# Kernel optimization log

Measured on AMD Instinct MI355X. Metric: run time of the kernel, lower is better.

The kernel has to match this reference:

```python
import jax, jax.numpy as jnp
import numpy as np

N = 50000      # nodes
E = 640000     # edges
F_IN = 64      # node feature dim
H = 128        # hidden channels
G = 256        # graphs in batch
NEG_SLOPE = 0.2
BN_EPS = 1e-5


def setup_inputs() -> dict:
    key = jax.random.key(0)
    ks = jax.random.split(key, 32)
    rn = lambda k, shape, s=0.1: jax.random.normal(k, shape, dtype=jnp.float32) * s
    inp = {
        'x': jax.random.normal(ks[0], (N, F_IN), dtype=jnp.float32),
        'edge_index': jax.random.randint(ks[1], (2, E), 0, N, dtype=jnp.int32),
        'batch': jnp.sort(jax.random.randint(ks[2], (N,), 0, G, dtype=jnp.int32)),
        # GATConv 1
        'W1': rn(ks[3], (F_IN, H)), 'as1': rn(ks[4], (H,)), 'ad1': rn(ks[5], (H,)), 'b1': jnp.zeros((H,), jnp.float32),
        # GATConv 2
        'W2': rn(ks[6], (H, H)), 'as2': rn(ks[7], (H,)), 'ad2': rn(ks[8], (H,)), 'b2': jnp.zeros((H,), jnp.float32),
        # GATConv 3
        'W3': rn(ks[9], (H, H)), 'as3': rn(ks[10], (H,)), 'ad3': rn(ks[11], (H,)), 'b3': jnp.zeros((H,), jnp.float32),
        # BatchNorm (inference: running stats)
        'g1': jnp.ones((H,), jnp.float32), 'be1': jnp.zeros((H,), jnp.float32), 'm1': rn(ks[12], (H,), 0.01), 'v1': jnp.ones((H,), jnp.float32),
        'g2': jnp.ones((H,), jnp.float32), 'be2': jnp.zeros((H,), jnp.float32), 'm2': rn(ks[13], (H,), 0.01), 'v2': jnp.ones((H,), jnp.float32),
        'g3': jnp.ones((H,), jnp.float32), 'be3': jnp.zeros((H,), jnp.float32), 'm3': rn(ks[14], (H,), 0.01), 'v3': jnp.ones((H,), jnp.float32),
        # MLP head
        'lw1': rn(ks[15], (H, H)), 'lb1': jnp.zeros((H,), jnp.float32),
        'lw2': rn(ks[16], (H, 1)), 'lb2': jnp.zeros((1,), jnp.float32),
    }
    return inp


def gat_layer(x, src, dst, W, a_src, a_dst, b, n):
    # PyG GATConv, heads=1: linear, per-edge attention, segment softmax over dst, scatter-add.
    h = x @ W                                  # [N, H]
    s_src = h @ a_src                          # [N]
    s_dst = h @ a_dst                          # [N]
    e = jax.nn.leaky_relu(s_src[src] + s_dst[dst], NEG_SLOPE)   # [E']
    m = jax.ops.segment_max(e, dst, num_segments=n)
    ex = jnp.exp(e - m[dst])
    denom = jax.ops.segment_sum(ex, dst, num_segments=n)
    coef = ex / denom[dst]                     # softmax per destination node
    out = jax.ops.segment_sum(coef[:, None] * h[src], dst, num_segments=n)
    return out + b


def batch_norm(x, g, b, mean, var):
    return (x - mean) * jax.lax.rsqrt(var + BN_EPS) * g + b


def reference(x, edge_index, batch,
              W1, as1, ad1, b1, W2, as2, ad2, b2, W3, as3, ad3, b3,
              g1, be1, m1, v1, g2, be2, m2, v2, g3, be3, m3, v3,
              lw1, lb1, lw2, lb2):
    n = x.shape[0]
    loops = jnp.arange(n, dtype=edge_index.dtype)      # PyG adds self-loops by default
    src = jnp.concatenate([edge_index[0], loops])
    dst = jnp.concatenate([edge_index[1], loops])

    h = gat_layer(x, src, dst, W1, as1, ad1, b1, n)
    h = jax.nn.relu(batch_norm(h, g1, be1, m1, v1))
    h = gat_layer(h, src, dst, W2, as2, ad2, b2, n)
    h = jax.nn.relu(batch_norm(h, g2, be2, m2, v2))
    h = gat_layer(h, src, dst, W3, as3, ad3, b3, n)
    h = jax.nn.relu(batch_norm(h, g3, be3, m3, v3))

    # global_mean_pool
    counts = jax.ops.segment_sum(jnp.ones((n,), h.dtype), batch, num_segments=G)
    pooled = jax.ops.segment_sum(h, batch, num_segments=G) / jnp.maximum(counts, 1.0)[:, None]

    out = jax.nn.relu(pooled @ lw1 + lb1)
    out = out @ lw2 + lb2                               # [G, 1]
    return out
```

## Files before the change

kernel.cpp:

```cpp
#include <hip/hip_runtime.h>

#define HD 128
#define NEG 0.2f
#define BNEPS 1e-5f

typedef unsigned int uint32;
typedef __attribute__((ext_vector_type(8))) short short8;
typedef __attribute__((ext_vector_type(4))) float floatx4;


__device__ inline float wave_max_f(float v) {
#pragma unroll
  for (int off = 32; off; off >>= 1) v = fmaxf(v, __shfl_xor(v, off, 64));
  return v;
}
__device__ inline float wave_sum_f(float v) {
#pragma unroll
  for (int off = 32; off; off >>= 1) v += __shfl_xor(v, off, 64);
  return v;
}
__device__ inline int wave_sum_i(int v) {
#pragma unroll
  for (int off = 32; off; off >>= 1) v += __shfl_xor(v, off, 64);
  return v;
}
__device__ inline int wave_iscan_i(int v, int lane) {
#pragma unroll
  for (int off = 1; off < 64; off <<= 1) {
    int t = __shfl_up(v, off, 64);
    if (lane >= off) v += t;
  }
  return v;
}
__device__ inline uint32 f2bf(float f) {
  uint32 u = __float_as_uint(f);
  return (u + 0x7fffu + ((u >> 16) & 1u)) >> 16;
}
__device__ inline void kpair(int kc, int lg, int e2, bool perm, int& k_lo, int& k_hi) {
  if (!perm) {
    k_lo = kc * 32 + lg * 8 + e2 * 2;
    k_hi = k_lo + 1;
  } else {
    int w = kc * 16 + lg * 4 + e2;
    k_lo = ((w >> 4) << 5) + (w & 15);
    k_hi = k_lo + 16;
  }
}


__global__ void k_hist(const int* __restrict__ dst, int* __restrict__ deg, int E) {
  int i = blockIdx.x * blockDim.x + threadIdx.x;
  if (i < E) atomicAdd(&deg[dst[i]], 1);
}

__global__ __launch_bounds__(256) void k_scan_part(const int* __restrict__ deg,
                                                   int* __restrict__ part, int n) {
  const int t = threadIdx.x, lane = t & 63, wave = t >> 6;
  const int i = blockIdx.x * 256 + t;
  int v = (i < n) ? (deg[i] + 1) : 0;
  int wv = wave_sum_i(v);
  __shared__ int ws[4];
  if (lane == 0) ws[wave] = wv;
  __syncthreads();
  if (t == 0) part[blockIdx.x] = ws[0] + ws[1] + ws[2] + ws[3];
}

__global__ __launch_bounds__(256) void k_scan_part2(int* __restrict__ part, int nb) {
  const int t = threadIdx.x, lane = t & 63, wave = t >> 6;
  int v = (t < nb) ? part[t] : 0;
  int x = wave_iscan_i(v, lane);
  __shared__ int ws[4];
  if (lane == 63) ws[wave] = x;
  __syncthreads();
  int add = 0;
#pragma unroll
  for (int w = 0; w < 4; ++w)
    if (w < wave) add += ws[w];
  x += add;
  if (t < nb) part[t] = x;
}

__global__ __launch_bounds__(256) void k_scan_final(const int* __restrict__ deg,
                                                    const int* __restrict__ part,
                                                    int* __restrict__ offs,
                                                    int* __restrict__ csr,
                                                    int* __restrict__ cursor, int n) {
  const int t = threadIdx.x, lane = t & 63, wave = t >> 6;
  const int b = blockIdx.x;
  const int i = b * 256 + t;
  int v = (i < n) ? (deg[i] + 1) : 0;
  int x = wave_iscan_i(v, lane);
  __shared__ int ws[4];
  if (lane == 63) ws[wave] = x;
  __syncthreads();
  int add = (b > 0) ? part[b - 1] : 0;
#pragma unroll
  for (int w = 0; w < 4; ++w)
    if (w < wave) add += ws[w];
  x += add;
  if (i < n) {
    const int excl = x - v;
    offs[i + 1] = x;
    csr[excl] = i;
    cursor[i] = excl + 1;
  }
  if (i == 0) offs[0] = 0;
}

__global__ void k_fill_edges(const int* __restrict__ src, const int* __restrict__ dst,
                             int* __restrict__ cursor, int* __restrict__ csr, int E) {
  int i = blockIdx.x * blockDim.x + threadIdx.x;
  if (i < E) { int p = atomicAdd(&cursor[dst[i]], 1); csr[p] = src[i]; }
}

__global__ __launch_bounds__(256)
void k_pack(const float* __restrict__ W1, const float* __restrict__ as1v,
            const float* __restrict__ ad1v, const float* __restrict__ W2,
            const float* __restrict__ as2v, const float* __restrict__ ad2v,
            const float* __restrict__ W3, const float* __restrict__ as3v,
            const float* __restrict__ ad3v, uint32* __restrict__ PW1,
            uint32* __restrict__ PW2, uint32* __restrict__ PW3,
            uint32* __restrict__ BFA1, uint32* __restrict__ BFA2,
            uint32* __restrict__ BFA3) {
  const int b = blockIdx.x, t = threadIdx.x;
  if (b < 80) {
    const float* W;
    uint32* PW;
    int KC, local;
    bool perm;
    if (b < 16) { W = W1; PW = PW1; KC = 2; perm = false; local = b; }
    else if (b < 48) { W = W2; PW = PW2; KC = 4; perm = true; local = b - 16; }
    else { W = W3; PW = PW3; KC = 4; perm = true; local = b - 48; }
    const int idx = local * 256 + t;
    const int e2 = idx & 3, l = (idx >> 2) & 63, f = idx >> 8;
    const int kc = f % KC, ct = f / KC;
    int k_lo, k_hi;
    kpair(kc, l >> 4, e2, perm, k_lo, k_hi);
    const int col = ct * 16 + (l & 15);
    PW[idx] = f2bf(W[k_lo * HD + col]) | (f2bf(W[k_hi * HD + col]) << 16);
  } else {
    const int layer = b - 80;
    const float* W = layer == 0 ? W1 : layer == 1 ? W2 : W3;
    const float* av = layer == 0 ? as1v : layer == 1 ? as2v : as3v;
    const float* dv = layer == 0 ? ad1v : layer == 1 ? ad2v : ad3v;
    uint32* BFA = layer == 0 ? BFA1 : layer == 1 ? BFA2 : BFA3;
    const int K = layer == 0 ? 64 : 128, KC = K / 32;
    const bool perm = layer != 0;
    __shared__ float ws[128], wd[128];
    if (t < K) {
      float s = 0.f, d = 0.f;
      for (int j = 0; j < HD; ++j) {
        const float w = W[t * HD + j];
        s = fmaf(w, av[j], s);
        d = fmaf(w, dv[j], d);
      }
      ws[t] = s;
      wd[t] = d;
    }
    __syncthreads();
    const int total = KC * 256;
    for (int idx = t; idx < total; idx += 256) {
      const int e2 = idx & 3, l = (idx >> 2) & 63, kc = idx >> 8;
      int k_lo, k_hi;
      kpair(kc, l >> 4, e2, perm, k_lo, k_hi);
      const int li = l & 15;
      const float lo = li == 0 ? ws[k_lo] : li == 1 ? wd[k_lo] : 0.f;
      const float hi = li == 0 ? ws[k_hi] : li == 1 ? wd[k_hi] : 0.f;
      BFA[idx] = f2bf(lo) | (f2bf(hi) << 16);
    }
  }
}

template <int K, bool BF16IN>
__global__ __launch_bounds__(256)
void k_gemm_mfma(const void* __restrict__ Xv, const uint32* __restrict__ PW,
                 const uint32* __restrict__ BFA, uint32* __restrict__ Hh,
                 float* __restrict__ ssrc, float* __restrict__ sdst, int n) {
  constexpr int KC = K / 32;
  __shared__ uint32 Xl[64 * K / 2];
  const int t = threadIdx.x;
  const int wv = t >> 6, l = t & 63;
  const int rowbase = blockIdx.x * 64;

  short8 bfr[2][KC];
#pragma unroll
  for (int c2 = 0; c2 < 2; ++c2)
#pragma unroll
    for (int kc = 0; kc < KC; ++kc)
      bfr[c2][kc] = *((const short8*)PW + ((wv * 2 + c2) * KC + kc) * 64 + l);
  short8 bfa[KC];
  if (wv == 0) {
#pragma unroll
    for (int kc = 0; kc < KC; ++kc) bfa[kc] = *((const short8*)BFA + kc * 64 + l);
  }

  if (BF16IN) {
    const uint32* Xb = (const uint32*)Xv;
#pragma unroll
    for (int B = t; B < 64 * (K / 8); B += 256) {
      const int row = B / (K / 8), cb = B % (K / 8);
      const int r = min(rowbase + row, n - 1);
      const uint4 v = *(const uint4*)&Xb[(long)r * (K / 2) + cb * 4];
      *(uint4*)&Xl[row * (K / 2) + (cb ^ (row & 7)) * 4] = v;
    }
  } else {
    const float* X = (const float*)Xv;
    for (int i = t; i < 64 * (K / 4); i += 256) {
      const int row = i / (K / 4), kq = i % (K / 4);
      const int r = min(rowbase + row, n - 1);
      const float4 v = *(const float4*)&X[(long)r * K + kq * 4];
      uint2 p;
      p.x = f2bf(v.x) | (f2bf(v.y) << 16);
      p.y = f2bf(v.z) | (f2bf(v.w) << 16);
      int byte = row * (K * 2) + kq * 8;
      byte ^= (row & 7) << 4;
      *(uint2*)((char*)Xl + byte) = p;
    }
  }
  __syncthreads();

  floatx4 acc[4][2], acc2[4];
#pragma unroll
  for (int rt = 0; rt < 4; ++rt) {
    acc[rt][0] = (floatx4){0.f, 0.f, 0.f, 0.f};
    acc[rt][1] = (floatx4){0.f, 0.f, 0.f, 0.f};
    acc2[rt] = (floatx4){0.f, 0.f, 0.f, 0.f};
  }
  const int row_l = l & 15, kgrp = l >> 4;
#pragma unroll
  for (int rt = 0; rt < 4; ++rt) {
    const int row = rt * 16 + row_l;
#pragma unroll
    for (int kc = 0; kc < KC; ++kc) {
      const int byte = (row * (K * 2) + kc * 64 + kgrp * 16) ^ ((row & 7) << 4);
      const short8 af = *(const short8*)((const char*)Xl + byte);
      acc[rt][0] = __builtin_amdgcn_mfma_f32_16x16x32_bf16(af, bfr[0][kc], acc[rt][0], 0, 0, 0);
      acc[rt][1] = __builtin_amdgcn_mfma_f32_16x16x32_bf16(af, bfr[1][kc], acc[rt][1], 0, 0, 0);
      if (wv == 0)
        acc2[rt] = __builtin_amdgcn_mfma_f32_16x16x32_bf16(af, bfa[kc], acc2[rt], 0, 0, 0);
    }
  }

#pragma unroll
  for (int rt = 0; rt < 4; ++rt) {
#pragma unroll
    for (int r = 0; r < 4; ++r) {
      const int R = rowbase + rt * 16 + kgrp * 4 + r;
      if (R < n)
        Hh[(long)R * 64 + wv * 16 + row_l] =
            f2bf(acc[rt][0][r]) | (f2bf(acc[rt][1][r]) << 16);
    }
  }
  if (wv == 0 && row_l < 2) {
    float* tgt = (row_l == 0) ? ssrc : sdst;
#pragma unroll
    for (int rt = 0; rt < 4; ++rt)
#pragma unroll
      for (int r = 0; r < 4; ++r) {
        const int R = rowbase + rt * 16 + kgrp * 4 + r;
        if (R < n) tgt[R] = acc2[rt][r];
      }
  }
}

__global__ __launch_bounds__(256)
void k_agg(const uint32* __restrict__ Hh, const float* __restrict__ ssrc,
           const float* __restrict__ sdst, const int* __restrict__ offs,
           const int* __restrict__ csr, const float* __restrict__ bias,
           const float* __restrict__ gam, const float* __restrict__ bet,
           const float* __restrict__ mu, const float* __restrict__ var,
           uint32* __restrict__ Ybf, int n) {
  const int wid = (blockIdx.x * blockDim.x + threadIdx.x) >> 6;
  const int lane = threadIdx.x & 63;
  if (wid >= n) return;
  const int s0 = offs[wid], s1 = offs[wid + 1];
  const float sdv = sdst[wid];
  const int c0 = (lane >> 4) * 32 + (lane & 15);
  const int c1 = c0 + 16;
  float acc0 = 0.f, acc1 = 0.f, denom = 0.f, mx = -1e30f;
  for (int base = s0; base < s1; base += 64) {
    const int m = min(64, s1 - base);
    int sidx = 0;
    float e = -1e30f;
    if (lane < m) {
      sidx = csr[base + lane];
      float tt = ssrc[sidx] + sdv;
      e = (tt > 0.f) ? tt : NEG * tt;
    }
    const float cmx = wave_max_f(e);
    const float nmx = fmaxf(mx, cmx);
    if (nmx > mx) {
      const float sc = __expf(mx - nmx);
      acc0 *= sc; acc1 *= sc; denom *= sc;
      mx = nmx;
    }
    const float p = (lane < m) ? __expf(e - mx) : 0.f;
    denom += wave_sum_f(p);
    const uint32 pu = __float_as_uint(p);
    for (int jj = 0; jj < m; jj += 16) {
      int idxv[16];
      float wv[16];
#pragma unroll
      for (int u = 0; u < 16; ++u) {
        idxv[u] = __builtin_amdgcn_readlane(sidx, jj + u);
        wv[u] = __uint_as_float(__builtin_amdgcn_readlane(pu, jj + u));
      }
      uint32 g[16];
#pragma unroll
      for (int u = 0; u < 16; ++u) g[u] = Hh[(long)idxv[u] * 64 + lane];
#pragma unroll
      for (int u = 0; u < 16; ++u) {
        acc0 = fmaf(wv[u], __uint_as_float(g[u] << 16), acc0);
        acc1 = fmaf(wv[u], __uint_as_float(g[u] & 0xffff0000u), acc1);
      }
    }
  }
  const float inv = 1.f / denom;
  float v0 = acc0 * inv + bias[c0];
  float v1 = acc1 * inv + bias[c1];
  const float sc0 = gam[c0] * rsqrtf(var[c0] + BNEPS);
  const float sc1 = gam[c1] * rsqrtf(var[c1] + BNEPS);
  v0 = fmaxf((v0 - mu[c0]) * sc0 + bet[c0], 0.f);
  v1 = fmaxf((v1 - mu[c1]) * sc1 + bet[c1], 0.f);
  Ybf[(long)wid * 64 + lane] = f2bf(v0) | (f2bf(v1) << 16);
}

__global__ __launch_bounds__(256)
void k_pool_head(const uint32* __restrict__ Ybf, const int* __restrict__ batch, int n,
                 const float* __restrict__ lw1, const float* __restrict__ lb1,
                 const float* __restrict__ lw2, const float* __restrict__ lb2,
                 float* __restrict__ out) {
  const int g = blockIdx.x;
  const int wave = threadIdx.x >> 6, lane = threadIdx.x & 63;
  int lo = 0, hi = n;
  while (lo < hi) { int mid = (lo + hi) >> 1; if (batch[mid] < g) lo = mid + 1; else hi = mid; }
  const int start = lo;
  hi = n;
  while (lo < hi) { int mid = (lo + hi) >> 1; if (batch[mid] < g + 1) lo = mid + 1; else hi = mid; }
  const int end = lo;
  const int c0 = (lane >> 4) * 32 + (lane & 15);
  const int c1 = c0 + 16;
  float m0 = 0.f, m1 = 0.f;
  for (int i = start + wave; i < end; i += 4) {
    const uint32 gv = Ybf[(long)i * 64 + lane];
    m0 += __uint_as_float(gv << 16);
    m1 += __uint_as_float(gv & 0xffff0000u);
  }
  __shared__ float red[4][HD];
  red[wave][c0] = m0;
  red[wave][c1] = m1;
  __syncthreads();
  if (wave == 0) {
    m0 = red[0][c0] + red[1][c0] + red[2][c0] + red[3][c0];
    m1 = red[0][c1] + red[1][c1] + red[2][c1] + red[3][c1];
    const float cnt = (float)(end - start);
    const float invc = (cnt > 0.f) ? 1.f / cnt : 0.f;
    m0 *= invc;
    m1 *= invc;
    float t0 = lb1[c0], t1 = lb1[c1];
    for (int k = 0; k < HD; ++k) {
      const int srcl = ((k >> 5) << 4) + (k & 15);
      const float pv = __shfl(((k >> 4) & 1) ? m1 : m0, srcl, 64);
      t0 = fmaf(pv, lw1[k * HD + c0], t0);
      t1 = fmaf(pv, lw1[k * HD + c1], t1);
    }
    t0 = fmaxf(t0, 0.f);
    t1 = fmaxf(t1, 0.f);
    float p = t0 * lw2[c0] + t1 * lw2[c1];
#pragma unroll
    for (int off = 32; off; off >>= 1) p += __shfl_xor(p, off, 64);
    if (lane == 0) out[g] = p + lb2[0];
  }
}


extern "C" void kernel_launch(void* const* d_in, const int* in_sizes, int n_in,
                              void* d_out, int out_size, void* d_ws, size_t ws_size,
                              hipStream_t stream) {
  const float* x = (const float*)d_in[0];
  const int* ei = (const int*)d_in[1];
  const int* batch = (const int*)d_in[2];
  const float* W1 = (const float*)d_in[3];
  const float* as1 = (const float*)d_in[4];
  const float* ad1 = (const float*)d_in[5];
  const float* b1 = (const float*)d_in[6];
  const float* W2 = (const float*)d_in[7];
  const float* as2 = (const float*)d_in[8];
  const float* ad2 = (const float*)d_in[9];
  const float* b2 = (const float*)d_in[10];
  const float* W3 = (const float*)d_in[11];
  const float* as3 = (const float*)d_in[12];
  const float* ad3 = (const float*)d_in[13];
  const float* b3 = (const float*)d_in[14];
  const float* g1 = (const float*)d_in[15];
  const float* be1 = (const float*)d_in[16];
  const float* m1 = (const float*)d_in[17];
  const float* v1 = (const float*)d_in[18];
  const float* g2 = (const float*)d_in[19];
  const float* be2 = (const float*)d_in[20];
  const float* m2 = (const float*)d_in[21];
  const float* v2 = (const float*)d_in[22];
  const float* g3 = (const float*)d_in[23];
  const float* be3 = (const float*)d_in[24];
  const float* m3 = (const float*)d_in[25];
  const float* v3 = (const float*)d_in[26];
  const float* lw1 = (const float*)d_in[27];
  const float* lb1 = (const float*)d_in[28];
  const float* lw2 = (const float*)d_in[29];
  const float* lb2 = (const float*)d_in[30];

  const int n = in_sizes[0] / 64;
  const int E = in_sizes[1] / 2;
  const int* src = ei;
  const int* dst = ei + E;

  uint32* hbuf = (uint32*)d_ws;
  uint32* ybuf = hbuf + (long)n * 64;
  float* ssrc = (float*)(ybuf + (long)n * 64);
  float* sdstv = ssrc + n;
  int* deg = (int*)(sdstv + n);
  int* offs = deg + n;
  int* cursor = offs + n + 1;
  int* csr = cursor + n;
  int* part = csr + (E + n);
  uint32* PW1 = (uint32*)(part + 256);
  uint32* PW2 = PW1 + 4096;
  uint32* PW3 = PW2 + 8192;
  uint32* BFA1 = PW3 + 8192;
  uint32* BFA2 = BFA1 + 512;
  uint32* BFA3 = BFA2 + 1024;

  const int B = 256;
  dim3 blk(B);
  const int nb = (n + B - 1) / B;

  k_pack<<<dim3(83), blk, 0, stream>>>(W1, as1, ad1, W2, as2, ad2, W3, as3, ad3,
                                       PW1, PW2, PW3, BFA1, BFA2, BFA3);

  hipMemsetAsync(deg, 0, (size_t)n * sizeof(int), stream);
  k_hist<<<dim3((E + B - 1) / B), blk, 0, stream>>>(dst, deg, E);
  k_scan_part<<<dim3(nb), blk, 0, stream>>>(deg, part, n);
  k_scan_part2<<<dim3(1), blk, 0, stream>>>(part, nb);
  k_scan_final<<<dim3(nb), blk, 0, stream>>>(deg, part, offs, csr, cursor, n);
  k_fill_edges<<<dim3((E + B - 1) / B), blk, 0, stream>>>(src, dst, cursor, csr, E);

  const dim3 ggrid((n + 63) / 64);
  const dim3 agrid((n + 3) / 4);

  k_gemm_mfma<64, false><<<ggrid, blk, 0, stream>>>(x, PW1, BFA1, hbuf, ssrc, sdstv, n);
  k_agg<<<agrid, blk, 0, stream>>>(hbuf, ssrc, sdstv, offs, csr, b1, g1, be1, m1, v1, ybuf, n);
  k_gemm_mfma<128, true><<<ggrid, blk, 0, stream>>>(ybuf, PW2, BFA2, hbuf, ssrc, sdstv, n);
  k_agg<<<agrid, blk, 0, stream>>>(hbuf, ssrc, sdstv, offs, csr, b2, g2, be2, m2, v2, ybuf, n);
  k_gemm_mfma<128, true><<<ggrid, blk, 0, stream>>>(ybuf, PW3, BFA3, hbuf, ssrc, sdstv, n);
  k_agg<<<agrid, blk, 0, stream>>>(hbuf, ssrc, sdstv, offs, csr, b3, g3, be3, m3, v3, ybuf, n);

  k_pool_head<<<dim3(256), blk, 0, stream>>>(ybuf, batch, n, lw1, lb1, lw2, lb2,
                                             (float*)d_out);
}
```

Baseline: 242.6 us.

## Fuse CSR build into pack/GEMM launches and drop softmax max pass

Zeroing of degree counters moves into the weight-pack kernel, and the degree histogram runs as extra blocks of the first GEMM launch. The multi-kernel prefix scan is replaced by one kernel that allocates CSR segments with a global atomic, storing start/end pairs per node. The aggregation kernel drops the running-max softmax rescaling and exponentiates raw scores, and the gather loop is reorganized. This cuts launches and reduction work but risks exp overflow for large attention logits and changes CSR ordering.

```diff
diff --git a/kernel.cpp b/kernel.cpp
--- a/kernel.cpp
+++ b/kernel.cpp
@@ -9,17 +9,7 @@
 typedef __attribute__((ext_vector_type(4))) float floatx4;
 
 
-__device__ inline float wave_max_f(float v) {
-#pragma unroll
-  for (int off = 32; off; off >>= 1) v = fmaxf(v, __shfl_xor(v, off, 64));
-  return v;
-}
 __device__ inline float wave_sum_f(float v) {
-#pragma unroll
-  for (int off = 32; off; off >>= 1) v += __shfl_xor(v, off, 64);
-  return v;
-}
-__device__ inline int wave_sum_i(int v) {
 #pragma unroll
   for (int off = 32; off; off >>= 1) v += __shfl_xor(v, off, 64);
   return v;
@@ -47,72 +37,6 @@
   }
 }
 
-
-__global__ void k_hist(const int* __restrict__ dst, int* __restrict__ deg, int E) {
-  int i = blockIdx.x * blockDim.x + threadIdx.x;
-  if (i < E) atomicAdd(&deg[dst[i]], 1);
-}
-
-__global__ __launch_bounds__(256) void k_scan_part(const int* __restrict__ deg,
-                                                   int* __restrict__ part, int n) {
-  const int t = threadIdx.x, lane = t & 63, wave = t >> 6;
-  const int i = blockIdx.x * 256 + t;
-  int v = (i < n) ? (deg[i] + 1) : 0;
-  int wv = wave_sum_i(v);
-  __shared__ int ws[4];
-  if (lane == 0) ws[wave] = wv;
-  __syncthreads();
-  if (t == 0) part[blockIdx.x] = ws[0] + ws[1] + ws[2] + ws[3];
-}
-
-__global__ __launch_bounds__(256) void k_scan_part2(int* __restrict__ part, int nb) {
-  const int t = threadIdx.x, lane = t & 63, wave = t >> 6;
-  int v = (t < nb) ? part[t] : 0;
-  int x = wave_iscan_i(v, lane);
-  __shared__ int ws[4];
-  if (lane == 63) ws[wave] = x;
-  __syncthreads();
-  int add = 0;
-#pragma unroll
-  for (int w = 0; w < 4; ++w)
-    if (w < wave) add += ws[w];
-  x += add;
-  if (t < nb) part[t] = x;
-}
-
-__global__ __launch_bounds__(256) void k_scan_final(const int* __restrict__ deg,
-                                                    const int* __restrict__ part,
-                                                    int* __restrict__ offs,
-                                                    int* __restrict__ csr,
-                                                    int* __restrict__ cursor, int n) {
-  const int t = threadIdx.x, lane = t & 63, wave = t >> 6;
-  const int b = blockIdx.x;
-  const int i = b * 256 + t;
-  int v = (i < n) ? (deg[i] + 1) : 0;
-  int x = wave_iscan_i(v, lane);
-  __shared__ int ws[4];
-  if (lane == 63) ws[wave] = x;
-  __syncthreads();
-  int add = (b > 0) ? part[b - 1] : 0;
-#pragma unroll
-  for (int w = 0; w < 4; ++w)
-    if (w < wave) add += ws[w];
-  x += add;
-  if (i < n) {
-    const int excl = x - v;
-    offs[i + 1] = x;
-    csr[excl] = i;
-    cursor[i] = excl + 1;
-  }
-  if (i == 0) offs[0] = 0;
-}
-
-__global__ void k_fill_edges(const int* __restrict__ src, const int* __restrict__ dst,
-                             int* __restrict__ cursor, int* __restrict__ csr, int E) {
-  int i = blockIdx.x * blockDim.x + threadIdx.x;
-  if (i < E) { int p = atomicAdd(&cursor[dst[i]], 1); csr[p] = src[i]; }
-}
-
 __global__ __launch_bounds__(256)
 void k_pack(const float* __restrict__ W1, const float* __restrict__ as1v,
             const float* __restrict__ ad1v, const float* __restrict__ W2,
@@ -121,8 +45,15 @@
             const float* __restrict__ ad3v, uint32* __restrict__ PW1,
             uint32* __restrict__ PW2, uint32* __restrict__ PW3,
             uint32* __restrict__ BFA1, uint32* __restrict__ BFA2,
-            uint32* __restrict__ BFA3) {
+            uint32* __restrict__ BFA3, int* __restrict__ deg,
+            int* __restrict__ gcnt, int n) {
   const int b = blockIdx.x, t = threadIdx.x;
+  if (b >= 83) {
+    const int i = (b - 83) * 256 + t;
+    if (i < n) deg[i] = 0;
+    if (b == 83 && t == 0) gcnt[0] = 0;
+    return;
+  }
   if (b < 80) {
     const float* W;
     uint32* PW;
@@ -171,16 +102,49 @@
   }
 }
 
+__global__ __launch_bounds__(256)
+void k_alloc(const int* __restrict__ deg, int* __restrict__ gcnt,
+             int2* __restrict__ offs2, int* __restrict__ csr,
+             int* __restrict__ cursor, int n) {
+  const int t = threadIdx.x, lane = t & 63, wave = t >> 6;
+  const int i = blockIdx.x * 256 + t;
+  const int v = (i < n) ? deg[i] + 1 : 0;
+  const int x = wave_iscan_i(v, lane);
+  __shared__ int wsum[4];
+  __shared__ int bbase;
+  if (lane == 63) wsum[wave] = x;
+  __syncthreads();
+  if (t == 0) bbase = atomicAdd(gcnt, wsum[0] + wsum[1] + wsum[2] + wsum[3]);
+  __syncthreads();
+  int add = bbase;
+#pragma unroll
+  for (int w = 0; w < 4; ++w)
+    if (w < wave) add += wsum[w];
+  const int start = add + x - v;
+  if (i < n) {
+    offs2[i] = make_int2(start, start + v);
+    csr[start] = i;
+    cursor[i] = start + 1;
+  }
+}
+
+__global__ void k_fill_edges(const int* __restrict__ src, const int* __restrict__ dst,
+                             int* __restrict__ cursor, int* __restrict__ csr, int E) {
+  int i = blockIdx.x * blockDim.x + threadIdx.x;
+  if (i < E) { int p = atomicAdd(&cursor[dst[i]], 1); csr[p] = src[i]; }
+}
+
 template <int K, bool BF16IN>
-__global__ __launch_bounds__(256)
-void k_gemm_mfma(const void* __restrict__ Xv, const uint32* __restrict__ PW,
-                 const uint32* __restrict__ BFA, uint32* __restrict__ Hh,
-                 float* __restrict__ ssrc, float* __restrict__ sdst, int n) {
+__device__ inline void gemm_body(int bid, const void* __restrict__ Xv,
+                                 const uint32* __restrict__ PW,
+                                 const uint32* __restrict__ BFA,
+                                 uint32* __restrict__ Hh, float* __restrict__ ssrc,
+                                 float* __restrict__ sdst, int n) {
   constexpr int KC = K / 32;
   __shared__ uint32 Xl[64 * K / 2];
   const int t = threadIdx.x;
   const int wv = t >> 6, l = t & 63;
-  const int rowbase = blockIdx.x * 64;
+  const int rowbase = bid * 64;
 
   short8 bfr[2][KC];
 #pragma unroll
@@ -264,8 +228,30 @@
 }
 
 __global__ __launch_bounds__(256)
+void k_gemm1_hist(const void* __restrict__ Xv, const uint32* __restrict__ PW,
+                  const uint32* __restrict__ BFA, uint32* __restrict__ Hh,
+                  float* __restrict__ ssrc, float* __restrict__ sdst, int n,
+                  const int* __restrict__ dst, int* __restrict__ deg, int E, int GB) {
+  const int b = blockIdx.x;
+  if (b < GB) {
+    gemm_body<64, false>(b, Xv, PW, BFA, Hh, ssrc, sdst, n);
+  } else {
+    const int i = (b - GB) * 256 + threadIdx.x;
+    if (i < E) atomicAdd(&deg[dst[i]], 1);
+  }
+}
+
+template <int K>
+__global__ __launch_bounds__(256)
+void k_gemm_mfma(const void* __restrict__ Xv, const uint32* __restrict__ PW,
+                 const uint32* __restrict__ BFA, uint32* __restrict__ Hh,
+                 float* __restrict__ ssrc, float* __restrict__ sdst, int n) {
+  gemm_body<K, true>(blockIdx.x, Xv, PW, BFA, Hh, ssrc, sdst, n);
+}
+
+__global__ __launch_bounds__(256)
 void k_agg(const uint32* __restrict__ Hh, const float* __restrict__ ssrc,
-           const float* __restrict__ sdst, const int* __restrict__ offs,
+           const float* __restrict__ sdst, const int2* __restrict__ offs2,
            const int* __restrict__ csr, const float* __restrict__ bias,
            const float* __restrict__ gam, const float* __restrict__ bet,
            const float* __restrict__ mu, const float* __restrict__ var,
@@ -273,45 +259,39 @@
   const int wid = (blockIdx.x * blockDim.x + threadIdx.x) >> 6;
   const int lane = threadIdx.x & 63;
   if (wid >= n) return;
-  const int s0 = offs[wid], s1 = offs[wid + 1];
+  const int2 se = offs2[wid];
   const float sdv = sdst[wid];
   const int c0 = (lane >> 4) * 32 + (lane & 15);
   const int c1 = c0 + 16;
-  float acc0 = 0.f, acc1 = 0.f, denom = 0.f, mx = -1e30f;
-  for (int base = s0; base < s1; base += 64) {
-    const int m = min(64, s1 - base);
+  float acc0 = 0.f, acc1 = 0.f, denom = 0.f;
+  for (int base = se.x; base < se.y; base += 64) {
+    const int m = min(64, se.y - base);
     int sidx = 0;
-    float e = -1e30f;
+    float p = 0.f;
     if (lane < m) {
       sidx = csr[base + lane];
-      float tt = ssrc[sidx] + sdv;
-      e = (tt > 0.f) ? tt : NEG * tt;
-    }
-    const float cmx = wave_max_f(e);
-    const float nmx = fmaxf(mx, cmx);
-    if (nmx > mx) {
-      const float sc = __expf(mx - nmx);
-      acc0 *= sc; acc1 *= sc; denom *= sc;
-      mx = nmx;
-    }
-    const float p = (lane < m) ? __expf(e - mx) : 0.f;
+      const float tt = ssrc[sidx] + sdv;
+      const float e = (tt > 0.f) ? tt : NEG * tt;
+      p = __expf(e);
+    }
     denom += wave_sum_f(p);
     const uint32 pu = __float_as_uint(p);
     for (int jj = 0; jj < m; jj += 16) {
-      int idxv[16];
-      float wv[16];
+      uint32 g[16];
 #pragma unroll
       for (int u = 0; u < 16; ++u) {
-        idxv[u] = __builtin_amdgcn_readlane(sidx, jj + u);
-        wv[u] = __uint_as_float(__builtin_amdgcn_readlane(pu, jj + u));
+        if (jj + u < m) {
+          const int s = __builtin_amdgcn_readlane(sidx, jj + u);
+          g[u] = Hh[(long)s * 64 + lane];
+        }
       }
-      uint32 g[16];
-#pragma unroll
-      for (int u = 0; u < 16; ++u) g[u] = Hh[(long)idxv[u] * 64 + lane];
 #pragma unroll
       for (int u = 0; u < 16; ++u) {
-        acc0 = fmaf(wv[u], __uint_as_float(g[u] << 16), acc0);
-        acc1 = fmaf(wv[u], __uint_as_float(g[u] & 0xffff0000u), acc1);
+        if (jj + u < m) {
+          const float w = __uint_as_float(__builtin_amdgcn_readlane(pu, jj + u));
+          acc0 = fmaf(w, __uint_as_float(g[u] << 16), acc0);
+          acc1 = fmaf(w, __uint_as_float(g[u] & 0xffff0000u), acc1);
+        }
       }
     }
   }
@@ -419,11 +399,11 @@
   float* ssrc = (float*)(ybuf + (long)n * 64);
   float* sdstv = ssrc + n;
   int* deg = (int*)(sdstv + n);
-  int* offs = deg + n;
-  int* cursor = offs + n + 1;
+  int2* offs2 = (int2*)(deg + n);
+  int* cursor = (int*)(offs2 + n);
   int* csr = cursor + n;
-  int* part = csr + (E + n);
-  uint32* PW1 = (uint32*)(part + 256);
+  int* gcnt = csr + (E + n);
+  uint32* PW1 = (uint32*)(gcnt + 4);
   uint32* PW2 = PW1 + 4096;
   uint32* PW3 = PW2 + 8192;
   uint32* BFA1 = PW3 + 8192;
@@ -433,27 +413,23 @@
   const int B = 256;
   dim3 blk(B);
   const int nb = (n + B - 1) / B;
-
-  k_pack<<<dim3(83), blk, 0, stream>>>(W1, as1, ad1, W2, as2, ad2, W3, as3, ad3,
-                                       PW1, PW2, PW3, BFA1, BFA2, BFA3);
-
-  hipMemsetAsync(deg, 0, (size_t)n * sizeof(int), stream);
-  k_hist<<<dim3((E + B - 1) / B), blk, 0, stream>>>(dst, deg, E);
-  k_scan_part<<<dim3(nb), blk, 0, stream>>>(deg, part, n);
-  k_scan_part2<<<dim3(1), blk, 0, stream>>>(part, nb);
-  k_scan_final<<<dim3(nb), blk, 0, stream>>>(deg, part, offs, csr, cursor, n);
-  k_fill_edges<<<dim3((E + B - 1) / B), blk, 0, stream>>>(src, dst, cursor, csr, E);
-
-  const dim3 ggrid((n + 63) / 64);
+  const int eb = (E + B - 1) / B;
+  const int GB = (n + 63) / 64;
+
+  k_pack<<<dim3(83 + nb), blk, 0, stream>>>(W1, as1, ad1, W2, as2, ad2, W3, as3, ad3,
+                                            PW1, PW2, PW3, BFA1, BFA2, BFA3,
+                                            deg, gcnt, n);
+  k_gemm1_hist<<<dim3(GB + eb), blk, 0, stream>>>(x, PW1, BFA1, hbuf, ssrc, sdstv, n,
+                                                  dst, deg, E, GB);
+  k_alloc<<<dim3(nb), blk, 0, stream>>>(deg, gcnt, offs2, csr, cursor, n);
+  k_fill_edges<<<dim3(eb), blk, 0, stream>>>(src, dst, cursor, csr, E);
+
   const dim3 agrid((n + 3) / 4);
-
-  k_gemm_mfma<64, false><<<ggrid, blk, 0, stream>>>(x, PW1, BFA1, hbuf, ssrc, sdstv, n);
-  k_agg<<<agrid, blk, 0, stream>>>(hbuf, ssrc, sdstv, offs, csr, b1, g1, be1, m1, v1, ybuf, n);
-  k_gemm_mfma<128, true><<<ggrid, blk, 0, stream>>>(ybuf, PW2, BFA2, hbuf, ssrc, sdstv, n);
-  k_agg<<<agrid, blk, 0, stream>>>(hbuf, ssrc, sdstv, offs, csr, b2, g2, be2, m2, v2, ybuf, n);
-  k_gemm_mfma<128, true><<<ggrid, blk, 0, stream>>>(ybuf, PW3, BFA3, hbuf, ssrc, sdstv, n);
-  k_agg<<<agrid, blk, 0, stream>>>(hbuf, ssrc, sdstv, offs, csr, b3, g3, be3, m3, v3, ybuf, n);
-
+  k_agg<<<agrid, blk, 0, stream>>>(hbuf, ssrc, sdstv, offs2, csr, b1, g1, be1, m1, v1, ybuf, n);
+  k_gemm_mfma<128><<<dim3(GB), blk, 0, stream>>>(ybuf, PW2, BFA2, hbuf, ssrc, sdstv, n);
+  k_agg<<<agrid, blk, 0, stream>>>(hbuf, ssrc, sdstv, offs2, csr, b2, g2, be2, m2, v2, ybuf, n);
+  k_gemm_mfma<128><<<dim3(GB), blk, 0, stream>>>(ybuf, PW3, BFA3, hbuf, ssrc, sdstv, n);
+  k_agg<<<agrid, blk, 0, stream>>>(hbuf, ssrc, sdstv, offs2, csr, b3, g3, be3, m3, v3, ybuf, n);
   k_pool_head<<<dim3(256), blk, 0, stream>>>(ybuf, batch, n, lw1, lb1, lw2, lb2,
                                              (float*)d_out);
 }
```

Result: faster. 235.1 us (-3.1%).
